# Optimization experiments

Measured on AMD Instinct MI355X. Metric: run time of the kernel, lower is better.

Reference implementation:

```python
import jax, jax.numpy as jnp
import numpy as np

CK = 64  # key channels, used for the 1/sqrt(ck) scale


def setup_inputs() -> dict:
    key = jax.random.key(0)
    ks = jax.random.split(key, 9)
    B, C, D, H, W = 2, 64, 20, 20, 20
    ck = cv = co = 64
    s = 0.02
    return {
        "x": jax.random.normal(ks[0], (B, C, D, H, W), dtype=jnp.float32),
        "wq": jax.random.normal(ks[1], (ck, C), dtype=jnp.float32) * s,
        "bq": jax.random.normal(ks[2], (ck,), dtype=jnp.float32) * s,
        "wk": jax.random.normal(ks[3], (ck, C), dtype=jnp.float32) * s,
        "bk": jax.random.normal(ks[4], (ck,), dtype=jnp.float32) * s,
        "wv": jax.random.normal(ks[5], (cv, C), dtype=jnp.float32) * s,
        "bv": jax.random.normal(ks[6], (cv,), dtype=jnp.float32) * s,
        "wo": jax.random.normal(ks[7], (co, cv), dtype=jnp.float32) * s,
        "bo": jax.random.normal(ks[8], (co,), dtype=jnp.float32) * s,
    }


def reference(x, wq, bq, wk, bk, wv, bv, wo, bo):
    B, C, D, H, W = x.shape
    ck = wq.shape[0]
    cv = wv.shape[0]
    xf = x.reshape(B, C, -1)  # (B, C, N) with N = D*H*W
    # 1x1x1 convs == per-voxel channel matmuls
    q = jnp.einsum('kc,bcn->bnk', wq, xf) + bq           # (B, N, ck) queries (already transposed)
    k = jnp.einsum('kc,bcn->bkn', wk, xf) + bk[:, None]  # (B, ck, N) keys
    v = jnp.einsum('vc,bcn->bnv', wv, xf) + bv           # (B, N, cv) values (transposed)
    scale = 1.0 / jnp.sqrt(jnp.asarray(CK, dtype=x.dtype))
    attn = jax.nn.softmax(jnp.einsum('bnk,bkm->bnm', q, k) * scale, axis=-1)  # (B, N, N)
    # dropout is identity in eval mode
    out = jnp.einsum('bnm,bmv->bnv', attn, v)  # (B, N, cv)
    # faithful to torch: .view(batch, cv, d, h, w) reinterprets memory, no transpose
    out = out.reshape(B, cv, D, H, W)
    out = jnp.einsum('oc,bcdhw->bodhw', wo, out) + bo[None, :, None, None, None]
    return out
```

## Files before the change

### kernel.cpp

```cpp
#include <hip/hip_runtime.h>
#include <hip/hip_bf16.h>

typedef __bf16 bf16_t;
typedef __bf16 bf16x8 __attribute__((ext_vector_type(8)));
typedef float f32x4 __attribute__((ext_vector_type(4)));
typedef float f32x16 __attribute__((ext_vector_type(16)));

#define NV 8000
#define QB 125

#define GLOAD_LDS16(src, dst) \
    __builtin_amdgcn_global_load_lds((const __attribute__((address_space(1))) void*)(src), \
                                     (__attribute__((address_space(3))) void*)(dst), 16, 0, 0)

__device__ __forceinline__ bf16x8 cvt_bf16x8(const float* __restrict__ p) {
    float4 a = *reinterpret_cast<const float4*>(p);
    float4 b = *reinterpret_cast<const float4*>(p + 4);
    bf16x8 r;
    r[0] = (bf16_t)a.x; r[1] = (bf16_t)a.y; r[2] = (bf16_t)a.z; r[3] = (bf16_t)a.w;
    r[4] = (bf16_t)b.x; r[5] = (bf16_t)b.y; r[6] = (bf16_t)b.z; r[7] = (bf16_t)b.w;
    return r;
}

__device__ __forceinline__ unsigned pack2(float a, float b) {
    union { bf16_t h[2]; unsigned u; } x;
    x.h[0] = (bf16_t)a; x.h[1] = (bf16_t)b;
    return x.u;
}

__device__ __forceinline__ int sigma_of(int n) {
    int c = n / 125, a = n - 125 * c;
    return a * 64 + c;
}

__global__ __launch_bounds__(256) void qkv_kernel(
    const float* __restrict__ x,
    const float* __restrict__ wq, const float* __restrict__ bq,
    const float* __restrict__ wk, const float* __restrict__ bk,
    const float* __restrict__ wv, const float* __restrict__ bv,
    bf16_t* __restrict__ Q, bf16_t* __restrict__ Kr, bf16_t* __restrict__ Vt)
{
    __shared__ __align__(16) char xb[16 * 128];

    const int tid = threadIdx.x;
    const int b  = blockIdx.x / 500;
    const int n0 = (blockIdx.x % 500) * 16;

    {
        int c = tid >> 2, seg = tid & 3;
        float4 v4 = *reinterpret_cast<const float4*>(&x[((size_t)b * 64 + c) * NV + n0 + seg * 4]);
        #pragma unroll
        for (int j = 0; j < 4; ++j) {
            int vx = seg * 4 + j;
            *reinterpret_cast<bf16_t*>(xb + vx * 128 + ((c * 2) ^ ((vx & 7) << 4))) =
                (bf16_t)((&v4.x)[j]);
        }
    }
    __syncthreads();

    const int w  = tid >> 6;
    const int lane = tid & 63;
    const int g  = lane >> 4;
    const int lr = lane & 15;

    const bf16x8 xa0 = *reinterpret_cast<const bf16x8*>(
        xb + lr * 128 + ((16 * g) ^ ((lr & 7) << 4)));
    const bf16x8 xa1 = *reinterpret_cast<const bf16x8*>(
        xb + lr * 128 + ((64 + 16 * g) ^ ((lr & 7) << 4)));

    const f32x4 zero4 = {0.f, 0.f, 0.f, 0.f};
    const float QSCALE = 0.125f * 1.44269504088896f;
    const int kout = w * 16 + lr;

    {
        bf16x8 wb0 = cvt_bf16x8(wq + kout * 64 + 8 * g);
        bf16x8 wb1 = cvt_bf16x8(wq + kout * 64 + 32 + 8 * g);
        f32x4 acc = __builtin_amdgcn_mfma_f32_16x16x32_bf16(xa0, wb0, zero4, 0, 0, 0);
        acc = __builtin_amdgcn_mfma_f32_16x16x32_bf16(xa1, wb1, acc, 0, 0, 0);
        const float bias = bq[kout];
        #pragma unroll
        for (int j = 0; j < 4; ++j) {
            const int sig = sigma_of(n0 + 4 * g + j);
            Q[((size_t)b * NV + sig) * 64 + kout] = (bf16_t)((acc[j] + bias) * QSCALE);
        }
    }
    {
        bf16x8 wb0 = cvt_bf16x8(wk + kout * 64 + 8 * g);
        bf16x8 wb1 = cvt_bf16x8(wk + kout * 64 + 32 + 8 * g);
        f32x4 acc = __builtin_amdgcn_mfma_f32_16x16x32_bf16(xa0, wb0, zero4, 0, 0, 0);
        acc = __builtin_amdgcn_mfma_f32_16x16x32_bf16(xa1, wb1, acc, 0, 0, 0);
        const float bias = bk[kout];
        #pragma unroll
        for (int j = 0; j < 4; ++j)
            Kr[((size_t)b * NV + n0 + 4 * g + j) * 64 + kout] = (bf16_t)(acc[j] + bias);
    }
    {
        bf16x8 wb0 = cvt_bf16x8(wv + kout * 64 + 8 * g);
        bf16x8 wb1 = cvt_bf16x8(wv + kout * 64 + 32 + 8 * g);
        f32x4 acc = __builtin_amdgcn_mfma_f32_16x16x32_bf16(xa0, wb0, zero4, 0, 0, 0);
        acc = __builtin_amdgcn_mfma_f32_16x16x32_bf16(xa1, wb1, acc, 0, 0, 0);
        const float bias = bv[kout];
        union { uint2 u2; bf16_t h[4]; } pk;
        #pragma unroll
        for (int j = 0; j < 4; ++j) pk.h[j] = (bf16_t)(acc[j] + bias);
        *reinterpret_cast<uint2*>(&Vt[((size_t)b * 64 + kout) * NV + n0 + 4 * g]) = pk.u2;
    }
}

template<int S>
__global__ __launch_bounds__(256) void attn_kernel(
    const bf16_t* __restrict__ Q, const bf16_t* __restrict__ Kr,
    const bf16_t* __restrict__ Vt, float* __restrict__ Op, float* __restrict__ ml)
{
    __shared__ __align__(16) char kt[2][8192];
    __shared__ __align__(16) char vt[2][8192];
    __shared__ __align__(16) char pt[4][4096];

    const int tid  = threadIdx.x;
    const int s    = blockIdx.x % S;
    const int rem  = blockIdx.x / S;
    const int b    = rem / 63;
    const int qb   = rem % 63;
    const int q0   = qb * 128;
    const int t0   = (125 * s) / S;
    const int t1   = (125 * (s + 1)) / S;
    const int w    = tid >> 6;
    const int lane = tid & 63;
    const int lo   = lane & 31;
    const int hi   = lane >> 5;

    const int q  = q0 + w * 32 + lo;
    const int qc = q < NV ? q : NV - 1;

    bf16x8 bq[4];
    {
        const bf16_t* qrow = Q + ((size_t)b * NV + qc) * 64 + hi * 8;
        #pragma unroll
        for (int kk = 0; kk < 4; ++kk)
            bq[kk] = *reinterpret_cast<const bf16x8*>(qrow + kk * 16);
    }

    const char* kp = (const char*)(Kr + (size_t)b * NV * 64);
    const char* vp = (const char*)(Vt + (size_t)b * 64 * NV);

    const int srr = lane >> 3;
    const int sch = lane & 7;

    f32x16 acco[2]; acco[0] = f32x16{}; acco[1] = f32x16{};
    float m = -1e30f, l = 0.f;

    char* ptw = &pt[w][0] + lo * 128;
    const int swzq = (lo & 7) << 4;

    {
        const int m0 = t0 * 64;
        #pragma unroll
        for (int rnd = 0; rnd < 2; ++rnd) {
            const int r = w * 16 + rnd * 8 + srr;
            const int cb = (sch * 16) ^ ((r & 7) << 4);
            GLOAD_LDS16(kp + (size_t)(m0 + r) * 128 + cb, kt[0] + w * 2048 + rnd * 1024);
            GLOAD_LDS16(vp + (size_t)r * (NV * 2) + m0 * 2 + cb, vt[0] + w * 2048 + rnd * 1024);
        }
    }

    for (int t = t0; t < t1; ++t) {
        const int cur = (t - t0) & 1;
        __syncthreads();
        if (t + 1 < t1) {
            const int m0n = (t + 1) * 64;
            #pragma unroll
            for (int rnd = 0; rnd < 2; ++rnd) {
                const int r = w * 16 + rnd * 8 + srr;
                const int cb = (sch * 16) ^ ((r & 7) << 4);
                GLOAD_LDS16(kp + (size_t)(m0n + r) * 128 + cb, kt[cur ^ 1] + w * 2048 + rnd * 1024);
                GLOAD_LDS16(vp + (size_t)r * (NV * 2) + m0n * 2 + cb, vt[cur ^ 1] + w * 2048 + rnd * 1024);
            }
        }

        const char* ktb = kt[cur];
        f32x16 sa[2];
        #pragma unroll
        for (int kb = 0; kb < 2; ++kb) {
            const int krow = kb * 32 + lo;
            const int roff = krow * 128;
            const int swzk = (krow & 7) << 4;
            f32x16 acc{};
            #pragma unroll
            for (int kk = 0; kk < 4; ++kk) {
                const bf16x8 ka = *reinterpret_cast<const bf16x8*>(
                    ktb + roff + ((kk * 32 + hi * 16) ^ swzk));
                acc = __builtin_amdgcn_mfma_f32_32x32x16_bf16(ka, bq[kk], acc, 0, 0, 0);
            }
            sa[kb] = acc;
        }

        float mx = sa[0][0];
        #pragma unroll
        for (int r = 1; r < 16; ++r) mx = fmaxf(mx, sa[0][r]);
        #pragma unroll
        for (int r = 0; r < 16; ++r) mx = fmaxf(mx, sa[1][r]);
        mx = fmaxf(mx, __shfl_xor(mx, 32, 64));

        if (__any(mx > m + 8.0f)) {
            const float mn2 = fmaxf(m, mx);
            const float corr = exp2f(m - mn2);
            m = mn2;
            l *= corr;
            acco[0] *= corr;
            acco[1] *= corr;
        }

        float ps = 0.f;
        #pragma unroll
        for (int kb = 0; kb < 2; ++kb) {
            #pragma unroll
            for (int j = 0; j < 4; ++j) {
                float p0 = exp2f(sa[kb][4 * j + 0] - m);
                float p1 = exp2f(sa[kb][4 * j + 1] - m);
                float p2 = exp2f(sa[kb][4 * j + 2] - m);
                float p3 = exp2f(sa[kb][4 * j + 3] - m);
                ps += (p0 + p1) + (p2 + p3);
                uint2 pw;
                pw.x = pack2(p0, p1);
                pw.y = pack2(p2, p3);
                *reinterpret_cast<uint2*>(ptw + ((64 * kb + 16 * j + 8 * hi) ^ swzq)) = pw;
            }
        }
        ps += __shfl_xor(ps, 32, 64);
        l += ps;

        const char* vtb = vt[cur];
        #pragma unroll
        for (int ks = 0; ks < 4; ++ks) {
            union { uint4 u; bf16x8 v; } pf;
            pf.u = *reinterpret_cast<const uint4*>(ptw + ((ks * 32 + hi * 16) ^ swzq));
            #pragma unroll
            for (int vb = 0; vb < 2; ++vb) {
                const int vrow = vb * 32 + lo;
                const bf16x8 va = *reinterpret_cast<const bf16x8*>(
                    vtb + vrow * 128 + ((ks * 32 + hi * 16) ^ ((vrow & 7) << 4)));
                acco[vb] = __builtin_amdgcn_mfma_f32_32x32x16_bf16(va, pf.v, acco[vb], 0, 0, 0);
            }
        }
    }

    if (q < NV) {
        const size_t obase = ((size_t)(s * 2 + b) * NV + q) * 64;
        #pragma unroll
        for (int vb = 0; vb < 2; ++vb) {
            #pragma unroll
            for (int j = 0; j < 4; ++j) {
                f32x4 o4 = { acco[vb][4 * j + 0], acco[vb][4 * j + 1],
                             acco[vb][4 * j + 2], acco[vb][4 * j + 3] };
                *reinterpret_cast<f32x4*>(&Op[obase + vb * 32 + 8 * j + 4 * hi]) = o4;
            }
        }
        if (hi == 0) {
            float2 t2; t2.x = m; t2.y = l;
            *reinterpret_cast<float2*>(&ml[((size_t)(s * 2 + b) * NV + q) * 2]) = t2;
        }
    }
}

template<int S>
__global__ __launch_bounds__(256) void projc_kernel(
    const float* __restrict__ Op, const float* __restrict__ ml,
    const float* __restrict__ wo, const float* __restrict__ bo,
    float* __restrict__ out)
{
    __shared__ __align__(16) char bt[64 * 128];
    __shared__ float al[64 * 8];

    const int tid = threadIdx.x;
    const int b   = blockIdx.x / 125;
    const int a   = blockIdx.x % 125;

    if (tid < 64) {
        const int row = a * 64 + tid;
        float M = -1e30f;
        #pragma unroll
        for (int s = 0; s < S; ++s)
            M = fmaxf(M, ml[((size_t)(s * 2 + b) * NV + row) * 2]);
        float L = 0.f, av[S];
        #pragma unroll
        for (int s = 0; s < S; ++s) {
            const float mm = ml[((size_t)(s * 2 + b) * NV + row) * 2];
            const float ll = ml[((size_t)(s * 2 + b) * NV + row) * 2 + 1];
            const float aa = exp2f(mm - M);
            L += ll * aa;
            av[s] = aa;
        }
        const float inv = 1.0f / L;
        #pragma unroll
        for (int s = 0; s < S; ++s) al[tid * 8 + s] = av[s] * inv;
    }
    __syncthreads();

    {
        const int c = tid >> 2, sg = tid & 3;
        f32x4 acc[4] = {{0,0,0,0},{0,0,0,0},{0,0,0,0},{0,0,0,0}};
        #pragma unroll
        for (int s = 0; s < S; ++s) {
            const float fac = al[c * 8 + s];
            const float* base = &Op[((size_t)(s * 2 + b) * NV + a * 64 + c) * 64 + sg * 16];
            #pragma unroll
            for (int qq = 0; qq < 4; ++qq)
                acc[qq] += fac * *reinterpret_cast<const f32x4*>(base + qq * 4);
        }
        #pragma unroll
        for (int qq = 0; qq < 4; ++qq) {
            #pragma unroll
            for (int j = 0; j < 4; ++j) {
                const int v = sg * 16 + qq * 4 + j;
                *reinterpret_cast<bf16_t*>(bt + v * 128 + ((c * 2) ^ ((v & 7) << 4))) =
                    (bf16_t)acc[qq][j];
            }
        }
    }
    __syncthreads();

    const int w  = tid >> 6;
    const int lane = tid & 63;
    const int g  = lane >> 4;
    const int lr = lane & 15;

    const int orow = w * 16 + lr;
    const bf16x8 wa0 = cvt_bf16x8(wo + orow * 64 + 8 * g);
    const bf16x8 wa1 = cvt_bf16x8(wo + orow * 64 + 32 + 8 * g);
    const float4 bo4 = *reinterpret_cast<const float4*>(&bo[w * 16 + 4 * g]);

    const f32x4 zero4 = {0.f, 0.f, 0.f, 0.f};
    #pragma unroll
    for (int nf = 0; nf < 4; ++nf) {
        const int rrow = nf * 16 + lr;
        const bf16x8 gb0 = *reinterpret_cast<const bf16x8*>(
            bt + rrow * 128 + ((16 * g) ^ ((rrow & 7) << 4)));
        const bf16x8 gb1 = *reinterpret_cast<const bf16x8*>(
            bt + rrow * 128 + ((64 + 16 * g) ^ ((rrow & 7) << 4)));
        f32x4 acc = __builtin_amdgcn_mfma_f32_16x16x32_bf16(wa0, gb0, zero4, 0, 0, 0);
        acc = __builtin_amdgcn_mfma_f32_16x16x32_bf16(wa1, gb1, acc, 0, 0, 0);
        #pragma unroll
        for (int j = 0; j < 4; ++j) {
            const int o = w * 16 + 4 * g + j;
            out[((size_t)b * 64 + o) * NV + a * 64 + nf * 16 + lr] = acc[j] + (&bo4.x)[j];
        }
    }
}

extern "C" void kernel_launch(void* const* d_in, const int* in_sizes, int n_in,
                              void* d_out, int out_size, void* d_ws, size_t ws_size,
                              hipStream_t stream)
{
    const float* x  = (const float*)d_in[0];
    const float* wq = (const float*)d_in[1];
    const float* bq = (const float*)d_in[2];
    const float* wk = (const float*)d_in[3];
    const float* bk = (const float*)d_in[4];
    const float* wv = (const float*)d_in[5];
    const float* bv = (const float*)d_in[6];
    const float* wo = (const float*)d_in[7];
    const float* bo = (const float*)d_in[8];
    float* out = (float*)d_out;

    char* ws = (char*)d_ws;
    bf16_t* Q  = (bf16_t*)(ws);
    bf16_t* Kr = (bf16_t*)(ws + 2048000);
    bf16_t* Vt = (bf16_t*)(ws + 4096000);

    int S = 8;
    if (ws_size < 6144000ull + 8ull * 4224000ull) S = 4;
    if (ws_size < 6144000ull + 4ull * 4224000ull) S = 2;
    if (ws_size < 6144000ull + 2ull * 4224000ull) S = 1;

    float* Op = (float*)(ws + 6144000);
    float* ml = (float*)(ws + 6144000 + (size_t)S * 4096000);

    qkv_kernel<<<dim3(2 * 500), dim3(256), 0, stream>>>(x, wq, bq, wk, bk, wv, bv, Q, Kr, Vt);

    if (S == 8) {
        attn_kernel<8><<<dim3(8 * 2 * 63), dim3(256), 0, stream>>>(Q, Kr, Vt, Op, ml);
        projc_kernel<8><<<dim3(2 * 125), dim3(256), 0, stream>>>(Op, ml, wo, bo, out);
    } else if (S == 4) {
        attn_kernel<4><<<dim3(4 * 2 * 63), dim3(256), 0, stream>>>(Q, Kr, Vt, Op, ml);
        projc_kernel<4><<<dim3(2 * 125), dim3(256), 0, stream>>>(Op, ml, wo, bo, out);
    } else if (S == 2) {
        attn_kernel<2><<<dim3(2 * 2 * 63), dim3(256), 0, stream>>>(Q, Kr, Vt, Op, ml);
        projc_kernel<2><<<dim3(2 * 125), dim3(256), 0, stream>>>(Op, ml, wo, bo, out);
    } else {
        attn_kernel<1><<<dim3(1 * 2 * 63), dim3(256), 0, stream>>>(Q, Kr, Vt, Op, ml);
        projc_kernel<1><<<dim3(2 * 125), dim3(256), 0, stream>>>(Op, ml, wo, bo, out);
    }
}
```

Baseline: 170.7 us.

## Keep P in registers via permlane32 swap and pre-shuffle K/V LDS tiles

Drops the per-wave LDS round trip for the softmax probabilities. The packed bf16 P values are now rearranged into MFMA B-operand layout with permlane32_swap. K and V tiles are staged into LDS already in per-lane fragment order, so reads become contiguous lane*16 accesses with no XOR swizzle. The cross-half max and sum reductions also use permlane32_swap instead of shfl_xor. This cuts LDS traffic, LDS footprint and address arithmetic, but the new global-to-LDS loads fetch scattered 16-byte pieces, which may hurt global coalescing.

```diff
diff --git a/kernel.cpp b/kernel.cpp
--- a/kernel.cpp
+++ b/kernel.cpp
@@ -5,6 +5,7 @@
 typedef __bf16 bf16x8 __attribute__((ext_vector_type(8)));
 typedef float f32x4 __attribute__((ext_vector_type(4)));
 typedef float f32x16 __attribute__((ext_vector_type(16)));
+typedef unsigned uint2v __attribute__((ext_vector_type(2)));
 
 #define NV 8000
 #define QB 125
@@ -114,7 +115,6 @@
 {
     __shared__ __align__(16) char kt[2][8192];
     __shared__ __align__(16) char vt[2][8192];
-    __shared__ __align__(16) char pt[4][4096];
 
     const int tid  = threadIdx.x;
     const int s    = blockIdx.x % S;
@@ -143,63 +143,62 @@
     const char* kp = (const char*)(Kr + (size_t)b * NV * 64);
     const char* vp = (const char*)(Vt + (size_t)b * 64 * NV);
 
-    const int srr = lane >> 3;
-    const int sch = lane & 7;
-
     f32x16 acco[2]; acco[0] = f32x16{}; acco[1] = f32x16{};
     float m = -1e30f, l = 0.f;
 
-    char* ptw = &pt[w][0] + lo * 128;
-    const int swzq = (lo & 7) << 4;
-
-    {
-        const int m0 = t0 * 64;
-        #pragma unroll
-        for (int rnd = 0; rnd < 2; ++rnd) {
-            const int r = w * 16 + rnd * 8 + srr;
-            const int cb = (sch * 16) ^ ((r & 7) << 4);
-            GLOAD_LDS16(kp + (size_t)(m0 + r) * 128 + cb, kt[0] + w * 2048 + rnd * 1024);
-            GLOAD_LDS16(vp + (size_t)r * (NV * 2) + m0 * 2 + cb, vt[0] + w * 2048 + rnd * 1024);
-        }
-    }
+    #define STAGE_TILE(m0, kdst, vdst)                                                   \
+        _Pragma("unroll")                                                                \
+        for (int rr = 0; rr < 2; ++rr) {                                                 \
+            const int gk = w + 4 * rr;                                                   \
+            const int kb_ = gk >> 2, kk_ = gk & 3;                                       \
+            GLOAD_LDS16(kp + (size_t)((m0) + kb_ * 32 + lo) * 128 + kk_ * 32 + hi * 16,  \
+                        (kdst) + gk * 1024);                                             \
+            const int ks_ = gk >> 1, vb_ = gk & 1;                                       \
+            GLOAD_LDS16(vp + (size_t)(vb_ * 32 + lo) * (NV * 2)                          \
+                           + (size_t)((m0) + ks_ * 16 + hi * 8) * 2,                     \
+                        (vdst) + gk * 1024);                                             \
+        }
+
+    STAGE_TILE(t0 * 64, kt[0], vt[0]);
 
     for (int t = t0; t < t1; ++t) {
         const int cur = (t - t0) & 1;
         __syncthreads();
         if (t + 1 < t1) {
-            const int m0n = (t + 1) * 64;
-            #pragma unroll
-            for (int rnd = 0; rnd < 2; ++rnd) {
-                const int r = w * 16 + rnd * 8 + srr;
-                const int cb = (sch * 16) ^ ((r & 7) << 4);
-                GLOAD_LDS16(kp + (size_t)(m0n + r) * 128 + cb, kt[cur ^ 1] + w * 2048 + rnd * 1024);
-                GLOAD_LDS16(vp + (size_t)r * (NV * 2) + m0n * 2 + cb, vt[cur ^ 1] + w * 2048 + rnd * 1024);
-            }
+            STAGE_TILE((t + 1) * 64, kt[cur ^ 1], vt[cur ^ 1]);
         }
 
         const char* ktb = kt[cur];
         f32x16 sa[2];
         #pragma unroll
         for (int kb = 0; kb < 2; ++kb) {
-            const int krow = kb * 32 + lo;
-            const int roff = krow * 128;
-            const int swzk = (krow & 7) << 4;
             f32x16 acc{};
             #pragma unroll
             for (int kk = 0; kk < 4; ++kk) {
                 const bf16x8 ka = *reinterpret_cast<const bf16x8*>(
-                    ktb + roff + ((kk * 32 + hi * 16) ^ swzk));
+                    ktb + ((kb * 4 + kk) * 64 + lane) * 16);
                 acc = __builtin_amdgcn_mfma_f32_32x32x16_bf16(ka, bq[kk], acc, 0, 0, 0);
             }
             sa[kb] = acc;
         }
 
-        float mx = sa[0][0];
-        #pragma unroll
-        for (int r = 1; r < 16; ++r) mx = fmaxf(mx, sa[0][r]);
-        #pragma unroll
-        for (int r = 0; r < 16; ++r) mx = fmaxf(mx, sa[1][r]);
-        mx = fmaxf(mx, __shfl_xor(mx, 32, 64));
+        float mx;
+        {
+            float v8[8];
+            #pragma unroll
+            for (int r = 0; r < 8; ++r)
+                v8[r] = fmaxf(fmaxf(sa[0][r], sa[0][r + 8]),
+                              fmaxf(sa[1][r], sa[1][r + 8]));
+            float v4a = fmaxf(v8[0], v8[4]), v4b = fmaxf(v8[1], v8[5]);
+            float v4c = fmaxf(v8[2], v8[6]), v4d = fmaxf(v8[3], v8[7]);
+            mx = fmaxf(fmaxf(v4a, v4b), fmaxf(v4c, v4d));
+        }
+        {
+            union { float f; unsigned u; } xu; xu.f = mx;
+            uint2v r = __builtin_amdgcn_permlane32_swap(xu.u, xu.u, false, false);
+            union { unsigned u; float f; } po; po.u = hi ? r[0] : r[1];
+            mx = fmaxf(mx, po.f);
+        }
 
         if (__any(mx > m + 8.0f)) {
             const float mn2 = fmaxf(m, mx);
@@ -211,6 +210,7 @@
         }
 
         float ps = 0.f;
+        unsigned Uw[2][4][2];
         #pragma unroll
         for (int kb = 0; kb < 2; ++kb) {
             #pragma unroll
@@ -220,26 +220,37 @@
                 float p2 = exp2f(sa[kb][4 * j + 2] - m);
                 float p3 = exp2f(sa[kb][4 * j + 3] - m);
                 ps += (p0 + p1) + (p2 + p3);
-                uint2 pw;
-                pw.x = pack2(p0, p1);
-                pw.y = pack2(p2, p3);
-                *reinterpret_cast<uint2*>(ptw + ((64 * kb + 16 * j + 8 * hi) ^ swzq)) = pw;
+                Uw[kb][j][0] = pack2(p0, p1);
+                Uw[kb][j][1] = pack2(p2, p3);
             }
         }
-        ps += __shfl_xor(ps, 32, 64);
+        {
+            union { float f; unsigned u; } xu; xu.f = ps;
+            uint2v r = __builtin_amdgcn_permlane32_swap(xu.u, xu.u, false, false);
+            union { unsigned u; float f; } po; po.u = hi ? r[0] : r[1];
+            ps += po.f;
+        }
         l += ps;
 
         const char* vtb = vt[cur];
         #pragma unroll
-        for (int ks = 0; ks < 4; ++ks) {
-            union { uint4 u; bf16x8 v; } pf;
-            pf.u = *reinterpret_cast<const uint4*>(ptw + ((ks * 32 + hi * 16) ^ swzq));
-            #pragma unroll
-            for (int vb = 0; vb < 2; ++vb) {
-                const int vrow = vb * 32 + lo;
-                const bf16x8 va = *reinterpret_cast<const bf16x8*>(
-                    vtb + vrow * 128 + ((ks * 32 + hi * 16) ^ ((vrow & 7) << 4)));
-                acco[vb] = __builtin_amdgcn_mfma_f32_32x32x16_bf16(va, pf.v, acco[vb], 0, 0, 0);
+        for (int kb = 0; kb < 2; ++kb) {
+            #pragma unroll
+            for (int e = 0; e < 2; ++e) {
+                uint2v r0 = __builtin_amdgcn_permlane32_swap(
+                    Uw[kb][2 * e][0], Uw[kb][2 * e + 1][0], false, false);
+                uint2v r1 = __builtin_amdgcn_permlane32_swap(
+                    Uw[kb][2 * e][1], Uw[kb][2 * e + 1][1], false, false);
+                union { unsigned u[4]; bf16x8 v; } pf;
+                pf.u[0] = r0[0]; pf.u[1] = r1[0];
+                pf.u[2] = r0[1]; pf.u[3] = r1[1];
+                const int ks = kb * 2 + e;
+                #pragma unroll
+                for (int vb = 0; vb < 2; ++vb) {
+                    const bf16x8 va = *reinterpret_cast<const bf16x8*>(
+                        vtb + ((ks * 2 + vb) * 64 + lane) * 16);
+                    acco[vb] = __builtin_amdgcn_mfma_f32_32x32x16_bf16(va, pf.v, acco[vb], 0, 0, 0);
+                }
             }
         }
     }
@@ -260,6 +271,7 @@
             *reinterpret_cast<float2*>(&ml[((size_t)(s * 2 + b) * NV + q) * 2]) = t2;
         }
     }
+    #undef STAGE_TILE
 }
 
 template<int S>
```

Result: slower. 181.1 us (+6.1%).
